# Kernel tuning notes

Hardware: AMD Instinct MI355X
Metric: run time of the kernel (lower is better)

Reference implementation:

```python
import jax, jax.numpy as jnp
import numpy as np

N = 50000
E = 800000
IN = 128
H = 4
C = 32  # hidden_channels per head; H*C == 128 so every layer is 128->128
NEG_SLOPE = 0.2  # PyG GATConv default negative_slope


def setup_inputs() -> dict:
    key = jax.random.key(0)
    ks = jax.random.split(key, 20)
    inp = {
        "x": jax.random.normal(ks[0], (N, IN), dtype=jnp.float32),
        "edge_index": jax.random.randint(ks[1], (2, E), 0, N, dtype=jnp.int64),
    }
    # 4 GATConv layers, each 128 -> (H=4, C=32), concat -> 128
    for i in range(4):
        k = jax.random.split(ks[2 + i], 4)
        inp[f"W{i+1}"] = jax.random.normal(k[0], (IN, H * C), dtype=jnp.float32) * 0.08
        inp[f"as{i+1}"] = jax.random.normal(k[1], (H, C), dtype=jnp.float32) * 0.08
        inp[f"ad{i+1}"] = jax.random.normal(k[2], (H, C), dtype=jnp.float32) * 0.08
        inp[f"b{i+1}"] = jnp.zeros((H * C,), dtype=jnp.float32)
    return inp


def gat_conv(x, src, dst, W, a_src, a_dst, bias):
    n = x.shape[0]
    h = (x @ W).reshape(n, H, C)                       # [N,H,C]
    alpha_src = jnp.einsum("nhc,hc->nh", h, a_src)      # [N,H]
    alpha_dst = jnp.einsum("nhc,hc->nh", h, a_dst)      # [N,H]
    e = jax.nn.leaky_relu(alpha_src[src] + alpha_dst[dst], NEG_SLOPE)  # [E,H]
    # segment softmax over incoming edges of each dst node
    emax = jax.ops.segment_max(e, dst, num_segments=n)
    emax = jnp.where(jnp.isfinite(emax), emax, 0.0)
    ex = jnp.exp(e - emax[dst])
    denom = jax.ops.segment_sum(ex, dst, num_segments=n)
    alpha = ex / denom[dst]                             # [E,H]
    msg = h[src] * alpha[:, :, None]                    # [E,H,C]
    out = jax.ops.segment_sum(msg, dst, num_segments=n) # [N,H,C]
    return out.reshape(n, H * C) + bias


def reference(x, edge_index, W1, as1, ad1, b1, W2, as2, ad2, b2,
              W3, as3, ad3, b3, W4, as4, ad4, b4):
    # PyG GATConv add_self_loops=True: append self-loops once
    loops = jnp.arange(N, dtype=edge_index.dtype)
    src = jnp.concatenate([edge_index[0], loops])
    dst = jnp.concatenate([edge_index[1], loops])
    x1 = jax.nn.relu(gat_conv(x, src, dst, W1, as1, ad1, b1))
    x2 = jax.nn.relu(gat_conv(x1, src, dst, W2, as2, ad2, b2))
    x3 = jax.nn.relu(gat_conv(x2, src, dst, W3, as3, ad3, b3))
    x4 = gat_conv(x3, src, dst, W4, as4, ad4, b4)
    return x4
```

## Files before the change

kernel.cpp:

```cpp
#include <hip/hip_runtime.h>
#include <hip/hip_fp16.h>
#include <math.h>

#define NNODES 50000
#define NEDGES 800000
#define NTOT   (NNODES + NEDGES)
#define GROWS  192
#define DEGCAP 64
#define EPB    4096
#define NBLK1  ((NEDGES + EPB - 1) / EPB)
#define NBUCK  98
#define SUBCAP 96

typedef _Float16 half8 __attribute__((ext_vector_type(8)));
typedef _Float16 half4 __attribute__((ext_vector_type(4)));
typedef float    f32x4 __attribute__((ext_vector_type(4)));


__global__ __launch_bounds__(512) void bin1_kernel(const int* __restrict__ ei,
                                                   unsigned int* __restrict__ region,
                                                   int* __restrict__ cnt) {
  __shared__ int lcnt[NBUCK];
  int t = threadIdx.x, blk = blockIdx.x;
  for (int i = t; i < NBUCK; i += 512) lcnt[i] = 0;
  __syncthreads();
  int e0 = blk * EPB;
  #pragma unroll
  for (int q = 0; q < EPB / 512; ++q) {
    int e = e0 + q * 512 + t;
    if (e < NEDGES) {
      int src = ei[e];
      int dst = ei[NEDGES + e];
      int b = dst >> 9;
      int r = atomicAdd(&lcnt[b], 1);
      if (r < SUBCAP)
        region[((size_t)blk * NBUCK + b) * SUBCAP + r] =
            (unsigned int)src | ((unsigned int)(dst & 511) << 20);
    }
  }
  __syncthreads();
  for (int i = t; i < NBUCK; i += 512) cnt[blk * NBUCK + i] = min(lcnt[i], SUBCAP);
}


__global__ __launch_bounds__(1024) void bin2_kernel(const unsigned int* __restrict__ region,
                                                    const int* __restrict__ cnt,
                                                    int* __restrict__ counts,
                                                    unsigned short* __restrict__ adj) {
  __shared__ int cur[512];
  int t = threadIdx.x, b = blockIdx.x;
  int nodeBase = b << 9;
  if (t < 512) {
    cur[t] = 1;
    int node = nodeBase + t;
    if (node < NNODES) adj[(size_t)node * DEGCAP] = (unsigned short)node;
  }
  __syncthreads();
  int wave = t >> 6, lane = t & 63;
  for (int i = wave; i < NBLK1; i += 16) {
    int ci = cnt[i * NBUCK + b];
    const unsigned int* sub = region + ((size_t)i * NBUCK + b) * SUBCAP;
    for (int j = lane; j < ci; j += 64) {
      unsigned int u = sub[j];
      int dl  = (int)(u >> 20);
      int src = (int)(u & 0xFFFFF);
      int slot = atomicAdd(&cur[dl], 1);
      if (slot < DEGCAP)
        adj[(size_t)(nodeBase + dl) * DEGCAP + slot] = (unsigned short)src;
    }
  }
  __syncthreads();
  if (t < 512 && nodeBase + t < NNODES) counts[nodeBase + t] = cur[t];
}


__global__ __launch_bounds__(256) void wprep4_kernel(
    const float* __restrict__ W0, const float* __restrict__ W1,
    const float* __restrict__ W2, const float* __restrict__ W3,
    _Float16* __restrict__ hi, _Float16* __restrict__ lo) {
  int id = blockIdx.x * 256 + threadIdx.x;
  int l = id >> 14, o = id & 16383;
  const float* W = (l == 0) ? W0 : (l == 1) ? W1 : (l == 2) ? W2 : W3;
  int n = o >> 7, k = o & 127;
  float v = W[k * 128 + n];
  _Float16 h = (_Float16)v;
  hi[id] = h;
  lo[id] = (_Float16)(v - (float)h);
}


__global__ __launch_bounds__(384) void gemm_mfma_kernel(
    const float* __restrict__ X, const _Float16* __restrict__ Wthi,
    const _Float16* __restrict__ Wtlo,
    const float* __restrict__ a_src, const float* __restrict__ a_dst,
    _Float16* __restrict__ Hh, float* __restrict__ alps, float* __restrict__ alpd) {
  __shared__ _Float16 whi[128 * 136];
  __shared__ _Float16 wlo[128 * 136];
  int t = threadIdx.x;

  for (int i = t; i < 2048; i += 384) {
    int n = i >> 4, koff = (i & 15) * 8;
    *(half8*)&whi[n * 136 + koff] = *(const half8*)&Wthi[n * 128 + koff];
    *(half8*)&wlo[n * 136 + koff] = *(const half8*)&Wtlo[n * 128 + koff];
  }
  __syncthreads();

  int wave = t >> 6, lane = t & 63;
  int r0 = blockIdx.x * GROWS + wave * 32 + (lane & 15);
  int r1 = r0 + 16;
  int kg = (lane >> 4) * 8;
  bool v0 = r0 < NNODES, v1 = r1 < NNODES;

  f32x4 acc0[8], acc1[8];
  #pragma unroll
  for (int tl = 0; tl < 8; ++tl) {
    acc0[tl] = (f32x4){0.f, 0.f, 0.f, 0.f};
    acc1[tl] = (f32x4){0.f, 0.f, 0.f, 0.f};
  }

  #pragma unroll
  for (int kt = 0; kt < 4; ++kt) {
    int k0 = kt * 32 + kg;
    half8 bh0, bl0, bh1, bl1;
    if (v0) {
      const float* xp = X + (size_t)r0 * 128 + k0;
      float4 f0 = *(const float4*)xp;
      float4 f1 = *(const float4*)(xp + 4);
      float fv[8] = {f0.x, f0.y, f0.z, f0.w, f1.x, f1.y, f1.z, f1.w};
      #pragma unroll
      for (int j = 0; j < 8; ++j) {
        _Float16 h = (_Float16)fv[j];
        bh0[j] = h;
        bl0[j] = (_Float16)(fv[j] - (float)h);
      }
    } else {
      #pragma unroll
      for (int j = 0; j < 8; ++j) { bh0[j] = (_Float16)0.f; bl0[j] = (_Float16)0.f; }
    }
    if (v1) {
      const float* xp = X + (size_t)r1 * 128 + k0;
      float4 f0 = *(const float4*)xp;
      float4 f1 = *(const float4*)(xp + 4);
      float fv[8] = {f0.x, f0.y, f0.z, f0.w, f1.x, f1.y, f1.z, f1.w};
      #pragma unroll
      for (int j = 0; j < 8; ++j) {
        _Float16 h = (_Float16)fv[j];
        bh1[j] = h;
        bl1[j] = (_Float16)(fv[j] - (float)h);
      }
    } else {
      #pragma unroll
      for (int j = 0; j < 8; ++j) { bh1[j] = (_Float16)0.f; bl1[j] = (_Float16)0.f; }
    }
    #pragma unroll
    for (int tl = 0; tl < 8; ++tl) {
      int aoff = (tl * 16 + (lane & 15)) * 136 + k0;
      half8 ah = *(const half8*)&whi[aoff];
      half8 al = *(const half8*)&wlo[aoff];
      acc0[tl] = __builtin_amdgcn_mfma_f32_16x16x32_f16(ah, bh0, acc0[tl], 0, 0, 0);
      acc0[tl] = __builtin_amdgcn_mfma_f32_16x16x32_f16(ah, bl0, acc0[tl], 0, 0, 0);
      acc0[tl] = __builtin_amdgcn_mfma_f32_16x16x32_f16(al, bh0, acc0[tl], 0, 0, 0);
      acc1[tl] = __builtin_amdgcn_mfma_f32_16x16x32_f16(ah, bh1, acc1[tl], 0, 0, 0);
      acc1[tl] = __builtin_amdgcn_mfma_f32_16x16x32_f16(ah, bl1, acc1[tl], 0, 0, 0);
      acc1[tl] = __builtin_amdgcn_mfma_f32_16x16x32_f16(al, bh1, acc1[tl], 0, 0, 0);
    }
  }

  int cg = (lane >> 4) * 4;
  #pragma unroll
  for (int g = 0; g < 2; ++g) {
    int row = (g == 0) ? r0 : r1;
    bool valid = (g == 0) ? v0 : v1;
    f32x4* acc = (g == 0) ? acc0 : acc1;
    float ps[4] = {0.f, 0.f, 0.f, 0.f}, pd[4] = {0.f, 0.f, 0.f, 0.f};
    #pragma unroll
    for (int tl = 0; tl < 8; ++tl) {
      int col0 = tl * 16 + cg;
      float4 as4 = *(const float4*)&a_src[col0];
      float4 ad4 = *(const float4*)&a_dst[col0];
      int hd = tl >> 1;
      ps[hd] += acc[tl][0] * as4.x + acc[tl][1] * as4.y + acc[tl][2] * as4.z + acc[tl][3] * as4.w;
      pd[hd] += acc[tl][0] * ad4.x + acc[tl][1] * ad4.y + acc[tl][2] * ad4.z + acc[tl][3] * ad4.w;
      if (valid) {
        half4 hv;
        hv[0] = (_Float16)acc[tl][0]; hv[1] = (_Float16)acc[tl][1];
        hv[2] = (_Float16)acc[tl][2]; hv[3] = (_Float16)acc[tl][3];
        *(half4*)&Hh[(size_t)row * 128 + col0] = hv;
      }
    }
    #pragma unroll
    for (int hd = 0; hd < 4; ++hd) {
      ps[hd] += __shfl_xor(ps[hd], 16, 64);
      ps[hd] += __shfl_xor(ps[hd], 32, 64);
      pd[hd] += __shfl_xor(pd[hd], 16, 64);
      pd[hd] += __shfl_xor(pd[hd], 32, 64);
    }
    if (valid && lane < 16) {
      *(f32x4*)&alps[row * 4] = (f32x4){ps[0], ps[1], ps[2], ps[3]};
      *(f32x4*)&alpd[row * 4] = (f32x4){pd[0], pd[1], pd[2], pd[3]};
    }
  }
}


#define AGG_BODY(JB)                                                    \
  {                                                                     \
    int jj = (JB) + e4;                                                 \
    int sj = s_lds[wslot][jj];                                          \
    float pj = p_lds[wslot][jj * 4 + hd_b];                             \
    const half8 hv = *(const half8*)(&Hh[(size_t)sj * 128 + col0]);     \
    a0 = fmaf(pj, (float)hv[0], a0);                                    \
    a1 = fmaf(pj, (float)hv[1], a1);                                    \
    a2 = fmaf(pj, (float)hv[2], a2);                                    \
    a3 = fmaf(pj, (float)hv[3], a3);                                    \
    a4 = fmaf(pj, (float)hv[4], a4);                                    \
    a5 = fmaf(pj, (float)hv[5], a5);                                    \
    a6 = fmaf(pj, (float)hv[6], a6);                                    \
    a7 = fmaf(pj, (float)hv[7], a7);                                    \
  }

__global__ __launch_bounds__(256) void agg_kernel(
    const _Float16* __restrict__ Hh, const float* __restrict__ alps,
    const float* __restrict__ alpd, const int* __restrict__ counts,
    const unsigned short* __restrict__ adj, const float* __restrict__ bias,
    float* __restrict__ out, int relu_flag) {
  __shared__ float p_lds[4][68 * 4];
  __shared__ int   s_lds[4][68];
  int wslot = threadIdx.x >> 6;
  int wid = (blockIdx.x * 256 + threadIdx.x) >> 6;
  if (wid >= NNODES) return;
  int lane = threadIdx.x & 63;
  int e4   = lane >> 4;
  int cidx = lane & 15;
  int hd_b = cidx >> 2;
  int col0 = cidx * 8;
  int nc = min(counts[wid], DEGCAP);

  float4 adv = *(const float4*)(&alpd[wid * 4]);

  float p0 = 0.f, p1 = 0.f, p2 = 0.f, p3 = 0.f;
  int src = 0;
  if (lane < nc) {
    src = (int)adj[(size_t)wid * DEGCAP + lane];
    float4 av = *(const float4*)(&alps[src * 4]);
    float v0 = av.x + adv.x, v1 = av.y + adv.y;
    float v2 = av.z + adv.z, v3 = av.w + adv.w;
    float e0 = (v0 > 0.f) ? v0 : 0.2f * v0;
    float e1 = (v1 > 0.f) ? v1 : 0.2f * v1;
    float e2v = (v2 > 0.f) ? v2 : 0.2f * v2;
    float e3 = (v3 > 0.f) ? v3 : 0.2f * v3;
    p0 = __expf(fminf(e0, 60.f));
    p1 = __expf(fminf(e1, 60.f));
    p2 = __expf(fminf(e2v, 60.f));
    p3 = __expf(fminf(e3, 60.f));
  }
  s_lds[wslot][lane] = src;
  *(float4*)(&p_lds[wslot][lane * 4]) = make_float4(p0, p1, p2, p3);
  if (lane < 4) {
    s_lds[wslot][64 + lane] = 0;
    *(float4*)(&p_lds[wslot][(64 + lane) * 4]) = make_float4(0.f, 0.f, 0.f, 0.f);
  }
  float q0 = p0, q1 = p1, q2 = p2, q3 = p3;
  #pragma unroll
  for (int off = 1; off < 64; off <<= 1) {
    q0 += __shfl_xor(q0, off, 64);
    q1 += __shfl_xor(q1, off, 64);
    q2 += __shfl_xor(q2, off, 64);
    q3 += __shfl_xor(q3, off, 64);
  }
  asm volatile("s_waitcnt lgkmcnt(0)" ::: "memory");

  float a0 = 0.f, a1 = 0.f, a2 = 0.f, a3 = 0.f;
  float a4 = 0.f, a5 = 0.f, a6 = 0.f, a7 = 0.f;
  int j = 0;
  for (; j + 16 <= nc; j += 16) {
    AGG_BODY(j) AGG_BODY(j + 4) AGG_BODY(j + 8) AGG_BODY(j + 12)
  }
  if (j + 8 <= nc) {
    AGG_BODY(j) AGG_BODY(j + 4)
    j += 8;
  }
  if (j < nc) {
    AGG_BODY(j) AGG_BODY(j + 4)
  }

  #pragma unroll
  for (int off = 16; off < 64; off <<= 1) {
    a0 += __shfl_xor(a0, off, 64);
    a1 += __shfl_xor(a1, off, 64);
    a2 += __shfl_xor(a2, off, 64);
    a3 += __shfl_xor(a3, off, 64);
    a4 += __shfl_xor(a4, off, 64);
    a5 += __shfl_xor(a5, off, 64);
    a6 += __shfl_xor(a6, off, 64);
    a7 += __shfl_xor(a7, off, 64);
  }

  if (lane < 16) {
    float sh = (hd_b == 0) ? q0 : (hd_b == 1) ? q1 : (hd_b == 2) ? q2 : q3;
    float inv = 1.0f / sh;
    float4 bv0 = *(const float4*)(&bias[col0]);
    float4 bv1 = *(const float4*)(&bias[col0 + 4]);
    float o0 = a0 * inv + bv0.x, o1 = a1 * inv + bv0.y;
    float o2 = a2 * inv + bv0.z, o3 = a3 * inv + bv0.w;
    float o4 = a4 * inv + bv1.x, o5 = a5 * inv + bv1.y;
    float o6 = a6 * inv + bv1.z, o7 = a7 * inv + bv1.w;
    if (relu_flag) {
      o0 = fmaxf(o0, 0.f); o1 = fmaxf(o1, 0.f); o2 = fmaxf(o2, 0.f); o3 = fmaxf(o3, 0.f);
      o4 = fmaxf(o4, 0.f); o5 = fmaxf(o5, 0.f); o6 = fmaxf(o6, 0.f); o7 = fmaxf(o7, 0.f);
    }
    *(float4*)(&out[(size_t)wid * 128 + col0])     = make_float4(o0, o1, o2, o3);
    *(float4*)(&out[(size_t)wid * 128 + col0 + 4]) = make_float4(o4, o5, o6, o7);
  }
}


extern "C" void kernel_launch(void* const* d_in, const int* in_sizes, int n_in,
                              void* d_out, int out_size, void* d_ws, size_t ws_size,
                              hipStream_t stream) {
  const float* x  = (const float*)d_in[0];
  const int*   ei = (const int*)d_in[1];
  const float* W[4]  = {(const float*)d_in[2],  (const float*)d_in[6],
                        (const float*)d_in[10], (const float*)d_in[14]};
  const float* As[4] = {(const float*)d_in[3],  (const float*)d_in[7],
                        (const float*)d_in[11], (const float*)d_in[15]};
  const float* Ad[4] = {(const float*)d_in[4],  (const float*)d_in[8],
                        (const float*)d_in[12], (const float*)d_in[16]};
  const float* Bs[4] = {(const float*)d_in[5],  (const float*)d_in[9],
                        (const float*)d_in[13], (const float*)d_in[17]};

  char* p = (char*)d_ws;
  auto alloc = [&](size_t bytes) {
    char* r = p;
    p += (bytes + 255) & ~(size_t)255;
    return r;
  };
  unsigned int*   region = (unsigned int*)alloc(sizeof(unsigned int) * (size_t)NBLK1 * NBUCK * SUBCAP);
  int*            cnt    = (int*)alloc(sizeof(int) * NBLK1 * NBUCK);
  int*            counts = (int*)alloc(sizeof(int) * NNODES);
  unsigned short* adj    = (unsigned short*)alloc(sizeof(unsigned short) * (size_t)NNODES * DEGCAP);
  float*          alps   = (float*)alloc(sizeof(float) * NNODES * 4);
  float*          alpd   = (float*)alloc(sizeof(float) * NNODES * 4);
  float*          bufA   = (float*)alloc(sizeof(float) * (size_t)NNODES * 128);
  _Float16*       Hh     = (_Float16*)alloc(sizeof(_Float16) * (size_t)NNODES * 128);
  _Float16*       Wthi   = (_Float16*)alloc(sizeof(_Float16) * 4 * 128 * 128);
  _Float16*       Wtlo   = (_Float16*)alloc(sizeof(_Float16) * 4 * 128 * 128);

  bin1_kernel  <<<NBLK1, 512, 0, stream>>>(ei, region, cnt);
  bin2_kernel  <<<NBUCK, 1024, 0, stream>>>(region, cnt, counts, adj);
  wprep4_kernel<<<256, 256, 0, stream>>>(W[0], W[1], W[2], W[3], Wthi, Wtlo);

  const float* cur = x;
  for (int l = 0; l < 4; ++l) {
    gemm_mfma_kernel<<<(NNODES + GROWS - 1) / GROWS, 384, 0, stream>>>(
        cur, Wthi + l * 16384, Wtlo + l * 16384, As[l], Ad[l], Hh, alps, alpd);
    float* o = (l == 3) ? (float*)d_out : bufA;
    agg_kernel<<<(NNODES * 64 + 255) / 256, 256, 0, stream>>>(
        Hh, alps, alpd, counts, adj, Bs[l], o, (l < 3) ? 1 : 0);
    cur = o;
  }
}
```

Measured before the change: 283.2 us.

## Store inter-layer activations in fp16 and merge weight prep into binning kernel

The hidden activations between layers are now written by the aggregation kernel as fp16 instead of fp32. The following GEMM then reads them directly as half8, with no split into hi/lo parts and one third fewer MFMAs per tile. The weight hi/lo preparation is folded into the binning kernel as extra blocks, which removes one launch. The aim is to halve activation traffic and cut GEMM compute, at the cost of the precision lost when intermediate activations are rounded to fp16.

Measured after the change: 262.4 us. 1.08x faster.

```diff
diff --git a/kernel.cpp b/kernel.cpp
--- a/kernel.cpp
+++ b/kernel.cpp
@@ -9,6 +9,7 @@
 #define DEGCAP 64
 #define EPB    4096
 #define NBLK1  ((NEDGES + EPB - 1) / EPB)
+#define NWPREP 32
 #define NBUCK  98
 #define SUBCAP 96
 
@@ -19,9 +20,30 @@
 
 __global__ __launch_bounds__(512) void bin1_kernel(const int* __restrict__ ei,
                                                    unsigned int* __restrict__ region,
-                                                   int* __restrict__ cnt) {
+                                                   int* __restrict__ cnt,
+                                                   const float* __restrict__ W0,
+                                                   const float* __restrict__ W1,
+                                                   const float* __restrict__ W2,
+                                                   const float* __restrict__ W3,
+                                                   _Float16* __restrict__ whi,
+                                                   _Float16* __restrict__ wlo) {
+  int t = threadIdx.x, blk = blockIdx.x;
+  if (blk >= NBLK1) {
+    int base = (blk - NBLK1) * 2048;
+    #pragma unroll
+    for (int q = 0; q < 4; ++q) {
+      int id = base + q * 512 + t;
+      int l = id >> 14, o = id & 16383;
+      const float* W = (l == 0) ? W0 : (l == 1) ? W1 : (l == 2) ? W2 : W3;
+      int n = o >> 7, k = o & 127;
+      float v = W[k * 128 + n];
+      _Float16 h = (_Float16)v;
+      whi[id] = h;
+      wlo[id] = (_Float16)(v - (float)h);
+    }
+    return;
+  }
   __shared__ int lcnt[NBUCK];
-  int t = threadIdx.x, blk = blockIdx.x;
   for (int i = t; i < NBUCK; i += 512) lcnt[i] = 0;
   __syncthreads();
   int e0 = blk * EPB;
@@ -74,24 +96,10 @@
 }
 
 
-__global__ __launch_bounds__(256) void wprep4_kernel(
-    const float* __restrict__ W0, const float* __restrict__ W1,
-    const float* __restrict__ W2, const float* __restrict__ W3,
-    _Float16* __restrict__ hi, _Float16* __restrict__ lo) {
-  int id = blockIdx.x * 256 + threadIdx.x;
-  int l = id >> 14, o = id & 16383;
-  const float* W = (l == 0) ? W0 : (l == 1) ? W1 : (l == 2) ? W2 : W3;
-  int n = o >> 7, k = o & 127;
-  float v = W[k * 128 + n];
-  _Float16 h = (_Float16)v;
-  hi[id] = h;
-  lo[id] = (_Float16)(v - (float)h);
-}
-
-
+template <bool XF16>
 __global__ __launch_bounds__(384) void gemm_mfma_kernel(
-    const float* __restrict__ X, const _Float16* __restrict__ Wthi,
-    const _Float16* __restrict__ Wtlo,
+    const float* __restrict__ X32, const _Float16* __restrict__ X16,
+    const _Float16* __restrict__ Wthi, const _Float16* __restrict__ Wtlo,
     const float* __restrict__ a_src, const float* __restrict__ a_dst,
     _Float16* __restrict__ Hh, float* __restrict__ alps, float* __restrict__ alpd) {
   __shared__ _Float16 whi[128 * 136];
@@ -122,35 +130,46 @@
   for (int kt = 0; kt < 4; ++kt) {
     int k0 = kt * 32 + kg;
     half8 bh0, bl0, bh1, bl1;
-    if (v0) {
-      const float* xp = X + (size_t)r0 * 128 + k0;
-      float4 f0 = *(const float4*)xp;
-      float4 f1 = *(const float4*)(xp + 4);
-      float fv[8] = {f0.x, f0.y, f0.z, f0.w, f1.x, f1.y, f1.z, f1.w};
-      #pragma unroll
-      for (int j = 0; j < 8; ++j) {
-        _Float16 h = (_Float16)fv[j];
-        bh0[j] = h;
-        bl0[j] = (_Float16)(fv[j] - (float)h);
+    if (XF16) {
+      if (v0) {
+        bh0 = *(const half8*)(X16 + (size_t)r0 * 128 + k0);
+      } else {
+        for (int j = 0; j < 8; ++j) bh0[j] = (_Float16)0.f;
+      }
+      if (v1) {
+        bh1 = *(const half8*)(X16 + (size_t)r1 * 128 + k0);
+      } else {
+        for (int j = 0; j < 8; ++j) bh1[j] = (_Float16)0.f;
       }
     } else {
-      #pragma unroll
-      for (int j = 0; j < 8; ++j) { bh0[j] = (_Float16)0.f; bl0[j] = (_Float16)0.f; }
-    }
-    if (v1) {
-      const float* xp = X + (size_t)r1 * 128 + k0;
-      float4 f0 = *(const float4*)xp;
-      float4 f1 = *(const float4*)(xp + 4);
-      float fv[8] = {f0.x, f0.y, f0.z, f0.w, f1.x, f1.y, f1.z, f1.w};
-      #pragma unroll
-      for (int j = 0; j < 8; ++j) {
-        _Float16 h = (_Float16)fv[j];
-        bh1[j] = h;
-        bl1[j] = (_Float16)(fv[j] - (float)h);
-      }
-    } else {
-      #pragma unroll
-      for (int j = 0; j < 8; ++j) { bh1[j] = (_Float16)0.f; bl1[j] = (_Float16)0.f; }
+      if (v0) {
+        const float* xp = X32 + (size_t)r0 * 128 + k0;
+        float4 f0 = *(const float4*)xp;
+        float4 f1 = *(const float4*)(xp + 4);
+        float fv[8] = {f0.x, f0.y, f0.z, f0.w, f1.x, f1.y, f1.z, f1.w};
+        #pragma unroll
+        for (int j = 0; j < 8; ++j) {
+          _Float16 h = (_Float16)fv[j];
+          bh0[j] = h;
+          bl0[j] = (_Float16)(fv[j] - (float)h);
+        }
+      } else {
+        for (int j = 0; j < 8; ++j) { bh0[j] = (_Float16)0.f; bl0[j] = (_Float16)0.f; }
+      }
+      if (v1) {
+        const float* xp = X32 + (size_t)r1 * 128 + k0;
+        float4 f0 = *(const float4*)xp;
+        float4 f1 = *(const float4*)(xp + 4);
+        float fv[8] = {f0.x, f0.y, f0.z, f0.w, f1.x, f1.y, f1.z, f1.w};
+        #pragma unroll
+        for (int j = 0; j < 8; ++j) {
+          _Float16 h = (_Float16)fv[j];
+          bh1[j] = h;
+          bl1[j] = (_Float16)(fv[j] - (float)h);
+        }
+      } else {
+        for (int j = 0; j < 8; ++j) { bh1[j] = (_Float16)0.f; bl1[j] = (_Float16)0.f; }
+      }
     }
     #pragma unroll
     for (int tl = 0; tl < 8; ++tl) {
@@ -158,11 +177,13 @@
       half8 ah = *(const half8*)&whi[aoff];
       half8 al = *(const half8*)&wlo[aoff];
       acc0[tl] = __builtin_amdgcn_mfma_f32_16x16x32_f16(ah, bh0, acc0[tl], 0, 0, 0);
-      acc0[tl] = __builtin_amdgcn_mfma_f32_16x16x32_f16(ah, bl0, acc0[tl], 0, 0, 0);
       acc0[tl] = __builtin_amdgcn_mfma_f32_16x16x32_f16(al, bh0, acc0[tl], 0, 0, 0);
       acc1[tl] = __builtin_amdgcn_mfma_f32_16x16x32_f16(ah, bh1, acc1[tl], 0, 0, 0);
-      acc1[tl] = __builtin_amdgcn_mfma_f32_16x16x32_f16(ah, bl1, acc1[tl], 0, 0, 0);
       acc1[tl] = __builtin_amdgcn_mfma_f32_16x16x32_f16(al, bh1, acc1[tl], 0, 0, 0);
+      if (!XF16) {
+        acc0[tl] = __builtin_amdgcn_mfma_f32_16x16x32_f16(ah, bl0, acc0[tl], 0, 0, 0);
+        acc1[tl] = __builtin_amdgcn_mfma_f32_16x16x32_f16(ah, bl1, acc1[tl], 0, 0, 0);
+      }
     }
   }
 
@@ -219,11 +240,12 @@
     a7 = fmaf(pj, (float)hv[7], a7);                                    \
   }
 
+template <bool OUTF16>
 __global__ __launch_bounds__(256) void agg_kernel(
     const _Float16* __restrict__ Hh, const float* __restrict__ alps,
     const float* __restrict__ alpd, const int* __restrict__ counts,
     const unsigned short* __restrict__ adj, const float* __restrict__ bias,
-    float* __restrict__ out, int relu_flag) {
+    float* __restrict__ out32, _Float16* __restrict__ out16, int relu_flag) {
   __shared__ float p_lds[4][68 * 4];
   __shared__ int   s_lds[4][68];
   int wslot = threadIdx.x >> 6;
@@ -309,8 +331,15 @@
       o0 = fmaxf(o0, 0.f); o1 = fmaxf(o1, 0.f); o2 = fmaxf(o2, 0.f); o3 = fmaxf(o3, 0.f);
       o4 = fmaxf(o4, 0.f); o5 = fmaxf(o5, 0.f); o6 = fmaxf(o6, 0.f); o7 = fmaxf(o7, 0.f);
     }
-    *(float4*)(&out[(size_t)wid * 128 + col0])     = make_float4(o0, o1, o2, o3);
-    *(float4*)(&out[(size_t)wid * 128 + col0 + 4]) = make_float4(o4, o5, o6, o7);
+    if (OUTF16) {
+      half8 hv;
+      hv[0] = (_Float16)o0; hv[1] = (_Float16)o1; hv[2] = (_Float16)o2; hv[3] = (_Float16)o3;
+      hv[4] = (_Float16)o4; hv[5] = (_Float16)o5; hv[6] = (_Float16)o6; hv[7] = (_Float16)o7;
+      *(half8*)(&out16[(size_t)wid * 128 + col0]) = hv;
+    } else {
+      *(float4*)(&out32[(size_t)wid * 128 + col0])     = make_float4(o0, o1, o2, o3);
+      *(float4*)(&out32[(size_t)wid * 128 + col0 + 4]) = make_float4(o4, o5, o6, o7);
+    }
   }
 }
 
@@ -341,22 +370,29 @@
   unsigned short* adj    = (unsigned short*)alloc(sizeof(unsigned short) * (size_t)NNODES * DEGCAP);
   float*          alps   = (float*)alloc(sizeof(float) * NNODES * 4);
   float*          alpd   = (float*)alloc(sizeof(float) * NNODES * 4);
-  float*          bufA   = (float*)alloc(sizeof(float) * (size_t)NNODES * 128);
+  _Float16*       actA   = (_Float16*)alloc(sizeof(_Float16) * (size_t)NNODES * 128);
   _Float16*       Hh     = (_Float16*)alloc(sizeof(_Float16) * (size_t)NNODES * 128);
   _Float16*       Wthi   = (_Float16*)alloc(sizeof(_Float16) * 4 * 128 * 128);
   _Float16*       Wtlo   = (_Float16*)alloc(sizeof(_Float16) * 4 * 128 * 128);
 
-  bin1_kernel  <<<NBLK1, 512, 0, stream>>>(ei, region, cnt);
-  bin2_kernel  <<<NBUCK, 1024, 0, stream>>>(region, cnt, counts, adj);
-  wprep4_kernel<<<256, 256, 0, stream>>>(W[0], W[1], W[2], W[3], Wthi, Wtlo);
-
-  const float* cur = x;
+  bin1_kernel<<<NBLK1 + NWPREP, 512, 0, stream>>>(ei, region, cnt,
+                                                  W[0], W[1], W[2], W[3], Wthi, Wtlo);
+  bin2_kernel<<<NBUCK, 1024, 0, stream>>>(region, cnt, counts, adj);
+
+  int ngemm = (NNODES + GROWS - 1) / GROWS;
+  int nagg  = (NNODES * 64 + 255) / 256;
   for (int l = 0; l < 4; ++l) {
-    gemm_mfma_kernel<<<(NNODES + GROWS - 1) / GROWS, 384, 0, stream>>>(
-        cur, Wthi + l * 16384, Wtlo + l * 16384, As[l], Ad[l], Hh, alps, alpd);
-    float* o = (l == 3) ? (float*)d_out : bufA;
-    agg_kernel<<<(NNODES * 64 + 255) / 256, 256, 0, stream>>>(
-        Hh, alps, alpd, counts, adj, Bs[l], o, (l < 3) ? 1 : 0);
-    cur = o;
-  }
-}
+    if (l == 0)
+      gemm_mfma_kernel<false><<<ngemm, 384, 0, stream>>>(
+          x, nullptr, Wthi + l * 16384, Wtlo + l * 16384, As[l], Ad[l], Hh, alps, alpd);
+    else
+      gemm_mfma_kernel<true><<<ngemm, 384, 0, stream>>>(
+          nullptr, actA, Wthi + l * 16384, Wtlo + l * 16384, As[l], Ad[l], Hh, alps, alpd);
+    if (l < 3)
+      agg_kernel<true><<<nagg, 256, 0, stream>>>(
+          Hh, alps, alpd, counts, adj, Bs[l], nullptr, actA, 1);
+    else
+      agg_kernel<false><<<nagg, 256, 0, stream>>>(
+          Hh, alps, alpd, counts, adj, Bs[l], (float*)d_out, nullptr, 0);
+  }
+}
```
